# Optimization experiments

Hardware: AMD Instinct MI355X
Metric: run time of the kernel (lower is better)

The kernel has to match this reference:

```python
import jax, jax.numpy as jnp
import numpy as np

N = 200000   # total atoms in batched graph
E = 3200000  # total bonds (directed edges)
B = 512      # number of graphs / sequences
L = 1000     # miRNA sequence length


def _gcn(x, W, b, src, dst, dis):
    # PyG GCNConv: add self-loops, symmetric normalization D^-1/2 A D^-1/2
    h = x @ W                                   # [N, Fout]
    msg = (dis[src] * dis[dst])[:, None] * h[src]
    agg = jax.ops.segment_sum(msg, dst, num_segments=x.shape[0])
    return agg + (dis * dis)[:, None] * h + b   # self-loop term + bias


def _conv1d(x, k, b):
    # x: [B, C, L], k: [O, I, K]  (torch Conv1d, VALID padding)
    y = jax.lax.conv_general_dilated(x, k, (1,), 'VALID',
                                     dimension_numbers=('NCH', 'OIH', 'NCH'))
    return y + b[None, :, None]


def _mp3(x):
    # torch MaxPool1d(3): window 3, stride 3, floor
    return jax.lax.reduce_window(x, -jnp.inf, jax.lax.max, (1, 1, 3), (1, 1, 3), 'VALID')


def setup_inputs() -> dict:
    key = jax.random.key(0)
    ks = jax.random.split(key, 24)
    w = lambda k, s: (jax.random.normal(k, s, jnp.float32) * 0.1)
    p = {}
    p['x'] = jax.random.normal(ks[0], (N, 4), jnp.float32)
    p['edge_index'] = jax.random.randint(ks[1], (2, E), 0, N, jnp.int32)
    p['batch'] = (jnp.arange(N, dtype=jnp.int32) * B // N).astype(jnp.int32)  # every graph non-empty
    p['target'] = jax.random.normal(ks[2], (B, L, 5), jnp.float32)
    # GCN layers 4->4->8->16
    p['W1'] = w(ks[3], (4, 4));    p['b1'] = jnp.zeros(4, jnp.float32)
    p['W2'] = w(ks[4], (4, 8));    p['b2'] = jnp.zeros(8, jnp.float32)
    p['W3'] = w(ks[5], (8, 16));   p['b3'] = jnp.zeros(16, jnp.float32)
    p['Wg1'] = w(ks[6], (16, 1024)); p['bg1'] = jnp.zeros(1024, jnp.float32)
    p['Wg2'] = w(ks[7], (1024, 128)); p['bg2'] = jnp.zeros(128, jnp.float32)
    # CNN stack on sequences, kernels [O, I, 8]
    p['K1'] = w(ks[8], (32, 5, 8));   p['cb1'] = jnp.zeros(32, jnp.float32)
    p['K2'] = w(ks[9], (64, 32, 8));  p['cb2'] = jnp.zeros(64, jnp.float32)
    p['K3'] = w(ks[10], (128, 64, 8)); p['cb3'] = jnp.zeros(128, jnp.float32)
    p['Wxt'] = w(ks[11], (128, 128)); p['bxt'] = jnp.zeros(128, jnp.float32)
    # fusion head
    p['Wf1'] = w(ks[12], (256, 1024)); p['bf1'] = jnp.zeros(1024, jnp.float32)
    p['Wf2'] = w(ks[13], (1024, 512)); p['bf2'] = jnp.zeros(512, jnp.float32)
    p['Wo'] = w(ks[14], (512, 2));     p['bo'] = jnp.zeros(2, jnp.float32)
    return p


def reference(x, edge_index, batch, target, W1, b1, W2, b2, W3, b3,
              Wg1, bg1, Wg2, bg2, K1, cb1, K2, cb2, K3, cb3,
              Wxt, bxt, Wf1, bf1, Wf2, bf2, Wo, bo):
    src, dst = edge_index[0], edge_index[1]
    deg = jax.ops.segment_sum(jnp.ones(src.shape[0], x.dtype), dst,
                              num_segments=x.shape[0]) + 1.0  # +1 self-loop
    dis = jax.lax.rsqrt(deg)
    # Graph branch (dropout is identity in eval)
    h = jax.nn.relu(_gcn(x, W1, b1, src, dst, dis))
    h = jax.nn.relu(_gcn(h, W2, b2, src, dst, dis))
    h = jax.nn.relu(_gcn(h, W3, b3, src, dst, dis))
    g = jax.ops.segment_max(h, batch, num_segments=B)  # global_max_pool
    g = jax.nn.relu(g @ Wg1 + bg1)
    g = g @ Wg2 + bg2
    # Sequence branch
    t = jnp.transpose(target, (0, 2, 1))  # [B, 5, L]
    c = _mp3(jax.nn.relu(_conv1d(t, K1, cb1)))
    c = _mp3(jax.nn.relu(_conv1d(c, K2, cb2)))
    c = _mp3(jax.nn.relu(_conv1d(c, K3, cb3)))
    c = jnp.mean(c, axis=2)               # [B, 128]
    c = jax.nn.relu(c @ Wxt + bxt)
    # Fusion head
    xc = jnp.concatenate([g, c], axis=1)  # [B, 256]
    xc = jax.nn.relu(xc @ Wf1 + bf1)
    xc = jax.nn.relu(xc @ Wf2 + bf2)
    return xc @ Wo + bo                    # [B, 2]
```

## Files before the change

### kernel.cpp

```cpp
#include <hip/hip_runtime.h>
#include <hip/hip_fp16.h>
#include <cstddef>

#define NA 200000
#define NE 3200000
#define NB 512
#define NBKT 256
#define BKTN 782
#define BKTCAP 16384
#define NEPB 3200

typedef _Float16 hv2 __attribute__((ext_vector_type(2)));
typedef _Float16 half8 __attribute__((ext_vector_type(8)));
typedef float floatx4 __attribute__((ext_vector_type(4)));
union UH2 { unsigned u; __half2 h; hv2 v; };
__device__ __forceinline__ float4 h4f(unsigned a, unsigned b) {
    UH2 x, y; x.u = a; y.u = b;
    float2 fa = __half22float2(x.h), fb = __half22float2(y.h);
    return make_float4(fa.x, fa.y, fb.x, fb.y);
}
__device__ __forceinline__ unsigned f2h(float a, float b) {
    UH2 r; r.h = __float22half2_rn(make_float2(a, b));
    return r.u;
}

__global__ void k_init(unsigned* g, int* gcursor,
                       float* gvec, const float* __restrict__ bg2,
                       float* xf2, const float* __restrict__ bf2,
                       float* xf1, const float* __restrict__ bf1,
                       const float* __restrict__ K2, const float* __restrict__ K3,
                       __half* __restrict__ Wt2, __half* __restrict__ Wt3) {
    int i = blockIdx.x * blockDim.x + threadIdx.x;
    if (i < NB * 16) g[i] = 0u;
    if (i < NBKT) gcursor[i] = i * BKTCAP;
    if (i < NB * 128) gvec[i] = bg2[i & 127];
    if (i < NB * 512) xf2[i] = bf2[i & 511];
    if (i < NB * 1024) xf1[i] = bf1[i & 1023];
    if (i < 64 * 32 * 8) {
        int o = i >> 8, rem = i & 255, c = rem >> 3, kk = rem & 7;
        Wt2[(o << 8) + (kk << 5) + c] = __float2half(K2[i]);
    }
    if (i < 128 * 64 * 8) {
        int o = i >> 9, rem = i & 511, c = rem >> 3, kk = rem & 7;
        Wt3[(o << 9) + (kk << 6) + c] = __float2half(K3[i]);
    }
}

template<int CIN, int COUT, int OBLK, int LIN, int PITCH, int POUT, int NTT>
__device__ __forceinline__ void dev_conv1(int b, int oy,
        const float* __restrict__ in, const float* __restrict__ Kw,
        const float* __restrict__ bias, __half* __restrict__ out) {
    constexpr int SPO = 256 / OBLK;
    constexpr int PT = (NTT < 4) ? NTT : 4;
    constexpr int NPASS = (NTT + PT - 1) / PT;
    __shared__ __align__(16) float s_in[CIN * PITCH];
    for (int idx = threadIdx.x; idx < CIN * PITCH; idx += 256) s_in[idx] = 0.f;
    __syncthreads();
    for (int idx = threadIdx.x; idx < LIN * CIN; idx += 256) {
        int p = idx / CIN, c = idx - p * CIN;
        s_in[c * PITCH + p] = in[(size_t)b * (LIN * CIN) + idx];
    }
    __syncthreads();
    int ol = threadIdx.x / SPO;
    int s  = threadIdx.x - ol * SPO;
    int o  = oy * OBLK + ol;
    float bo = bias[o];
    const float* wrow = Kw + (size_t)o * CIN * 8;
    for (int pass = 0; pass < NPASS; pass++) {
        float acc[PT][12];
#pragma unroll
        for (int tt = 0; tt < PT; tt++)
#pragma unroll
            for (int j = 0; j < 12; j++) acc[tt][j] = 0.f;
        bool vld[PT]; int tgs[PT];
#pragma unroll
        for (int tt = 0; tt < PT; tt++) {
            int ta = pass * PT + tt;
            int tg = s + SPO * ta;
            tgs[tt] = tg;
            vld[tt] = (ta < NTT) && (4 * tg < POUT);
        }
        for (int i = 0; i < CIN; i++) {
            float wa[8];
            const float4* wp = (const float4*)(wrow + (size_t)i * 8);
            *(float4*)&wa[0] = wp[0];
            *(float4*)&wa[4] = wp[1];
#pragma unroll
            for (int tt = 0; tt < PT; tt++) {
                if (vld[tt]) {
                    const float4* xr = (const float4*)&s_in[i * PITCH + 12 * tgs[tt]];
                    float xa[20];
#pragma unroll
                    for (int q = 0; q < 5; q++) *(float4*)&xa[4 * q] = xr[q];
#pragma unroll
                    for (int j = 0; j < 12; j++) {
                        float sm = acc[tt][j];
#pragma unroll
                        for (int k = 0; k < 8; k++) sm = fmaf(xa[j + k], wa[k], sm);
                        acc[tt][j] = sm;
                    }
                }
            }
        }
#pragma unroll
        for (int tt = 0; tt < PT; tt++) {
            if (vld[tt]) {
#pragma unroll
                for (int p = 0; p < 4; p++) {
                    int P = 4 * tgs[tt] + p;
                    if (P < POUT) {
                        float m = fmaxf(fmaxf(acc[tt][3 * p], acc[tt][3 * p + 1]), acc[tt][3 * p + 2]);
                        out[((size_t)b * COUT + o) * POUT + P] = __float2half(fmaxf(m + bo, 0.f));
                    }
                }
            }
        }
    }
}

__device__ __forceinline__ void dev_conv2_mfma(int b,
        const __half* __restrict__ pool1, const __half* __restrict__ Wt2,
        const float* __restrict__ cb2, __half* __restrict__ pool2t,
        char* smem) {
    __half* sT   = (__half*)smem;
    __half* outS = (__half*)smem;
    const __half* inp = pool1 + (size_t)b * (32 * 331);
    for (int idx = threadIdx.x; idx < 32 * 331; idx += 256) {
        int c = idx / 331;
        int p = idx - c * 331;
        sT[p * 40 + c] = inp[idx];
    }
    __syncthreads();
    int lane = threadIdx.x & 63, wv = threadIdx.x >> 6;
    int l15 = lane & 15, lg = lane >> 4;
    int mtBeg = wv * 5;
    int nmt = (wv == 3) ? 6 : 5;
    const floatx4 FZ = {0.f, 0.f, 0.f, 0.f};
    floatx4 acc[6][4];
#pragma unroll
    for (int mi = 0; mi < 6; mi++)
#pragma unroll
        for (int nt = 0; nt < 4; nt++) acc[mi][nt] = FZ;
    const half8* WB = (const half8*)Wt2;
    for (int s = 0; s < 8; s++) {
        half8 bfr[4];
#pragma unroll
        for (int nt = 0; nt < 4; nt++)
            bfr[nt] = WB[(nt * 16 + l15) * 32 + s * 4 + lg];
        half8 afr[6];
#pragma unroll
        for (int mi = 0; mi < 6; mi++) {
            if (mi < nmt) {
                int row = (mtBeg + mi) * 16 + l15 + s;
                afr[mi] = *(const half8*)(sT + row * 40 + lg * 8);
            }
        }
#pragma unroll
        for (int mi = 0; mi < 6; mi++) {
            if (mi < nmt) {
#pragma unroll
                for (int nt = 0; nt < 4; nt++)
                    acc[mi][nt] = __builtin_amdgcn_mfma_f32_16x16x32_f16(
                        afr[mi], bfr[nt], acc[mi][nt], 0, 0, 0);
            }
        }
    }
    __syncthreads();
    float bo[4];
#pragma unroll
    for (int nt = 0; nt < 4; nt++) bo[nt] = cb2[nt * 16 + l15];
#pragma unroll
    for (int mi = 0; mi < 6; mi++) {
        if (mi < nmt) {
#pragma unroll
            for (int nt = 0; nt < 4; nt++) {
                int o = nt * 16 + l15;
#pragma unroll
                for (int r = 0; r < 4; r++) {
                    int p = (mtBeg + mi) * 16 + lg * 4 + r;
                    float v = fmaxf(acc[mi][nt][r] + bo[nt], 0.f);
                    outS[p * 68 + o] = __float2half(v);
                }
            }
        }
    }
    __syncthreads();
    __half* op = pool2t + (size_t)b * (108 * 64);
    for (int idx = threadIdx.x; idx < 108 * 64; idx += 256) {
        int P = idx >> 6, o = idx & 63;
        float v0 = __half2float(outS[(3 * P) * 68 + o]);
        float v1 = __half2float(outS[(3 * P + 1) * 68 + o]);
        float v2 = __half2float(outS[(3 * P + 2) * 68 + o]);
        op[idx] = __float2half(fmaxf(fmaxf(v0, v1), v2));
    }
}

__device__ __forceinline__ void dev_conv3_mfma(int b,
        const __half* __restrict__ pool2t, const __half* __restrict__ Wt3,
        const float* __restrict__ cb3, float* __restrict__ pool3,
        char* smem) {
    __half* sT  = (__half*)smem;
    float* outS = (float*)smem;
    const uint4* inp = (const uint4*)(pool2t + (size_t)b * (108 * 64));
    for (int t = threadIdx.x; t < 108 * 8; t += 256) {
        int r = t >> 3, s8 = t & 7;
        *(uint4*)(sT + r * 72 + s8 * 8) = inp[t];
    }
    __syncthreads();
    int lane = threadIdx.x & 63, wv = threadIdx.x >> 6;
    int l15 = lane & 15, lg = lane >> 4;
    int mtBeg = wv * 2;
    int nmt = (wv == 3) ? 1 : 2;
    const floatx4 FZ = {0.f, 0.f, 0.f, 0.f};
    floatx4 acc[2][8];
#pragma unroll
    for (int mi = 0; mi < 2; mi++)
#pragma unroll
        for (int nt = 0; nt < 8; nt++) acc[mi][nt] = FZ;
    const half8* WB = (const half8*)Wt3;
    for (int s = 0; s < 16; s++) {
        half8 bfr[8];
#pragma unroll
        for (int nt = 0; nt < 8; nt++)
            bfr[nt] = WB[(nt * 16 + l15) * 64 + s * 4 + lg];
        half8 afr[2];
#pragma unroll
        for (int mi = 0; mi < 2; mi++) {
            if (mi < nmt) {
                int row = (mtBeg + mi) * 16 + l15 + (s >> 1);
                afr[mi] = *(const half8*)(sT + row * 72 + (s & 1) * 32 + lg * 8);
            }
        }
#pragma unroll
        for (int mi = 0; mi < 2; mi++) {
            if (mi < nmt) {
#pragma unroll
                for (int nt = 0; nt < 8; nt++)
                    acc[mi][nt] = __builtin_amdgcn_mfma_f32_16x16x32_f16(
                        afr[mi], bfr[nt], acc[mi][nt], 0, 0, 0);
            }
        }
    }
    __syncthreads();
    float bo[8];
#pragma unroll
    for (int nt = 0; nt < 8; nt++) bo[nt] = cb3[nt * 16 + l15];
#pragma unroll
    for (int mi = 0; mi < 2; mi++) {
        if (mi < nmt) {
#pragma unroll
            for (int nt = 0; nt < 8; nt++) {
                int o = nt * 16 + l15;
#pragma unroll
                for (int r = 0; r < 4; r++) {
                    int p = (mtBeg + mi) * 16 + lg * 4 + r;
                    if (p < 100)
                        outS[p * 132 + o] = fmaxf(acc[mi][nt][r] + bo[nt], 0.f);
                }
            }
        }
    }
    __syncthreads();
    float* op = pool3 + (size_t)b * (128 * 33);
    for (int idx = threadIdx.x; idx < 128 * 33; idx += 256) {
        int o = idx / 33, P = idx - o * 33;
        float v0 = outS[(3 * P) * 132 + o];
        float v1 = outS[(3 * P + 1) * 132 + o];
        float v2 = outS[(3 * P + 2) * 132 + o];
        op[idx] = fmaxf(fmaxf(v0, v1), v2);
    }
}

__global__ __launch_bounds__(256) void k_A(
        const int* __restrict__ src, const int* __restrict__ dst,
        int* __restrict__ gcursor, unsigned* __restrict__ stage,
        const float* __restrict__ tgt, const float* __restrict__ K1,
        const float* __restrict__ cb1, __half* __restrict__ pool1) {
    __shared__ int hcnt[NBKT];
    __shared__ int hbase[NBKT];
    int bx = blockIdx.x;
    if (bx >= 1000) {
        dev_conv1<5, 32, 16, 1000, 1008, 331, 6>(bx - 1000, 0, tgt, K1, cb1, pool1);
        return;
    }
    int e0 = bx * NEPB;
    hcnt[threadIdx.x] = 0;
    __syncthreads();
    const int4* d4 = (const int4*)(dst + e0);
    for (int i = threadIdx.x; i < NEPB / 4; i += 256) {
        int4 d = d4[i];
        atomicAdd(&hcnt[d.x / BKTN], 1);
        atomicAdd(&hcnt[d.y / BKTN], 1);
        atomicAdd(&hcnt[d.z / BKTN], 1);
        atomicAdd(&hcnt[d.w / BKTN], 1);
    }
    __syncthreads();
    hbase[threadIdx.x] = atomicAdd(&gcursor[threadIdx.x], hcnt[threadIdx.x]);
    hcnt[threadIdx.x] = 0;
    __syncthreads();
    const int4* s4 = (const int4*)(src + e0);
    for (int i = threadIdx.x; i < NEPB / 4; i += 256) {
        int4 d = d4[i];
        int4 s = s4[i];
        int ds[4] = {d.x, d.y, d.z, d.w};
        int ss[4] = {s.x, s.y, s.z, s.w};
#pragma unroll
        for (int j = 0; j < 4; j++) {
            int bkt = ds[j] / BKTN;
            int dloc = ds[j] - bkt * BKTN;
            int k = atomicAdd(&hcnt[bkt], 1);
            stage[hbase[bkt] + k] = ((unsigned)dloc << 18) | (unsigned)ss[j];
        }
    }
}

__global__ __launch_bounds__(256) void k_Bp(
        const unsigned* __restrict__ stage, const int* __restrict__ gcursor,
        int* __restrict__ rowptr, int* __restrict__ cnt, int* __restrict__ csr,
        const float* __restrict__ x, float4* __restrict__ dt1,
        const float* __restrict__ tgt, const float* __restrict__ K1,
        const float* __restrict__ cb1, __half* __restrict__ pool1) {
    __shared__ int lcnt[BKTN];
    __shared__ int lpos[BKTN];
    __shared__ int partial[256];
    __shared__ int sbase;
    int bx = blockIdx.x;
    if (bx >= NBKT) {
        dev_conv1<5, 32, 16, 1000, 1008, 331, 6>(bx - NBKT, 1, tgt, K1, cb1, pool1);
        return;
    }
    int t = threadIdx.x;
    int bkt = bx;
    int tot = gcursor[t] - t * BKTCAP;
    partial[t] = tot;
    __syncthreads();
#pragma unroll
    for (int off = 1; off < 256; off <<= 1) {
        int u = (t >= off) ? partial[t - off] : 0;
        __syncthreads();
        partial[t] += u;
        __syncthreads();
    }
    if (t == 0) sbase = (bkt == 0) ? 0 : partial[bkt - 1];
    __syncthreads();
    int base = sbase;
    int n0 = bkt * BKTN;
    int ncnt = (NA - n0 < BKTN) ? (NA - n0) : BKTN;
    int eBeg = bkt * BKTCAP;
    int eCnt = gcursor[bkt] - eBeg;
    for (int i = t; i < BKTN; i += 256) lcnt[i] = 0;
    __syncthreads();
    for (int i = t; i < eCnt; i += 256)
        atomicAdd(&lcnt[stage[eBeg + i] >> 18], 1);
    __syncthreads();
    int mysum = 0;
#pragma unroll
    for (int j = 0; j < 4; j++) {
        int node = 4 * t + j;
        if (node < ncnt) mysum += lcnt[node];
    }
    partial[t] = mysum;
    __syncthreads();
#pragma unroll
    for (int off = 1; off < 256; off <<= 1) {
        int u = (t >= off) ? partial[t - off] : 0;
        __syncthreads();
        partial[t] += u;
        __syncthreads();
    }
    int running = partial[t] - mysum;
#pragma unroll
    for (int j = 0; j < 4; j++) {
        int node = 4 * t + j;
        if (node < ncnt) {
            lpos[node] = running;
            rowptr[n0 + node] = base + running;
            cnt[n0 + node] = lcnt[node];
            running += lcnt[node];
        }
    }
    __syncthreads();
    for (int i = t; i < eCnt; i += 256) {
        unsigned v = stage[eBeg + i];
        int dloc = v >> 18;
        int s = v & 0x3FFFF;
        int k = atomicAdd(&lpos[dloc], 1);
        csr[base + k] = s;
    }
    for (int i = t; i < ncnt; i += 256) {
        int n = n0 + i;
        float4 p = ((const float4*)x)[n];
        float dv = rsqrtf((float)lcnt[i] + 1.0f);
        dt1[n] = make_float4(dv * p.x, dv * p.y, dv * p.z, dv * p.w);
    }
}

__global__ __launch_bounds__(256) void k_B(
        const __half* __restrict__ pool1, const __half* __restrict__ Wt2,
        const float* __restrict__ cb2, __half* __restrict__ pool2t,
        const float4* __restrict__ dt1, const int* __restrict__ rowptr,
        const int* __restrict__ cnt, const int* __restrict__ csr,
        const float* __restrict__ W1, const float* __restrict__ b1,
        float4* __restrict__ dt2) {
    __shared__ __align__(16) char smem[45696];
    int bx = blockIdx.x;
    if (bx < 512) {
        dev_conv2_mfma(bx, pool1, Wt2, cb2, pool2t, smem);
        return;
    }
    __shared__ float sW[16];
    if (threadIdx.x < 16) sW[threadIdx.x] = W1[threadIdx.x];
    __syncthreads();
    int n = (bx - 512) * 256 + threadIdx.x;
    if (n >= NA) return;
    int cn = cnt[n];
    float dv = rsqrtf((float)cn + 1.0f);
    const int* row = csr + rowptr[n];
    float4 acc = dt1[n];
    int e = 0;
    for (; e + 3 < cn; e += 4) {
        int i0 = row[e], i1 = row[e + 1], i2 = row[e + 2], i3 = row[e + 3];
        float4 v0 = dt1[i0], v1 = dt1[i1], v2 = dt1[i2], v3 = dt1[i3];
        acc.x += (v0.x + v1.x) + (v2.x + v3.x);
        acc.y += (v0.y + v1.y) + (v2.y + v3.y);
        acc.z += (v0.z + v1.z) + (v2.z + v3.z);
        acc.w += (v0.w + v1.w) + (v2.w + v3.w);
    }
    for (; e < cn; e++) {
        float4 v = dt1[row[e]];
        acc.x += v.x; acc.y += v.y; acc.z += v.z; acc.w += v.w;
    }
    const float4 bq = *(const float4*)b1;
    float a[4] = {acc.x, acc.y, acc.z, acc.w};
    float bb[4] = {bq.x, bq.y, bq.z, bq.w};
    float o[4];
#pragma unroll
    for (int f = 0; f < 4; f++) {
        float s = 0.f;
#pragma unroll
        for (int k = 0; k < 4; k++) s = fmaf(a[k], sW[k * 4 + f], s);
        o[f] = dv * fmaxf(fmaf(dv, s, bb[f]), 0.f);
    }
    dt2[n] = make_float4(o[0], o[1], o[2], o[3]);
}

__global__ __launch_bounds__(256) void k_C(
        const __half* __restrict__ pool2t, const __half* __restrict__ Wt3,
        const float* __restrict__ cb3, float* __restrict__ pool3,
        const float4* __restrict__ dt2, const int* __restrict__ rowptr,
        const int* __restrict__ cnt, const int* __restrict__ csr,
        const float* __restrict__ W2, const float* __restrict__ b2,
        uint4* __restrict__ dt3) {
    __shared__ __align__(16) char smem[52800];
    int bx = blockIdx.x;
    if (bx < 512) {
        dev_conv3_mfma(bx, pool2t, Wt3, cb3, pool3, smem);
        return;
    }
    __shared__ float sW[32];
    if (threadIdx.x < 32) sW[threadIdx.x] = W2[threadIdx.x];
    __syncthreads();
    int n = (bx - 512) * 256 + threadIdx.x;
    if (n >= NA) return;
    int cn = cnt[n];
    float dv = rsqrtf((float)cn + 1.0f);
    const int* row = csr + rowptr[n];
    float4 acc = dt2[n];
    int e = 0;
    for (; e + 3 < cn; e += 4) {
        int i0 = row[e], i1 = row[e + 1], i2 = row[e + 2], i3 = row[e + 3];
        float4 v0 = dt2[i0], v1 = dt2[i1], v2 = dt2[i2], v3 = dt2[i3];
        acc.x += (v0.x + v1.x) + (v2.x + v3.x);
        acc.y += (v0.y + v1.y) + (v2.y + v3.y);
        acc.z += (v0.z + v1.z) + (v2.z + v3.z);
        acc.w += (v0.w + v1.w) + (v2.w + v3.w);
    }
    for (; e < cn; e++) {
        float4 v = dt2[row[e]];
        acc.x += v.x; acc.y += v.y; acc.z += v.z; acc.w += v.w;
    }
    float a[4] = {acc.x, acc.y, acc.z, acc.w};
    float o[8];
#pragma unroll
    for (int f = 0; f < 8; f++) {
        float s = 0.f;
#pragma unroll
        for (int k = 0; k < 4; k++) s = fmaf(a[k], sW[k * 8 + f], s);
        o[f] = dv * fmaxf(fmaf(dv, s, b2[f]), 0.f);
    }
    dt3[n] = make_uint4(f2h(o[0], o[1]), f2h(o[2], o[3]),
                        f2h(o[4], o[5]), f2h(o[6], o[7]));
}

__global__ __launch_bounds__(256) void k_D(
        const uint4* __restrict__ dt3, const int* __restrict__ rowptr,
        const int* __restrict__ cnt, const int* __restrict__ csr,
        const float* __restrict__ W3, const float* __restrict__ b3,
        const int* __restrict__ batch, unsigned* __restrict__ g,
        const float* __restrict__ pool3, const float* __restrict__ Wxt,
        const float* __restrict__ bxt, float* __restrict__ cx) {
    int bx = blockIdx.x;
    if (bx >= 782) {
        __shared__ float sa[8 * 128];
        int b0 = (bx - 782) * 8;
        for (int t = threadIdx.x; t < 8 * 128; t += 256) {
            int gg = t >> 7, k = t & 127;
            const float* r = pool3 + ((size_t)(b0 + gg) * 128 + k) * 33;
            float s = 0.f;
#pragma unroll
            for (int p = 0; p < 33; p++) s += r[p];
            sa[t] = s * (1.f / 33.f);
        }
        __syncthreads();
        int j = threadIdx.x;
        if (j >= 128) return;
        float bj = bxt[j];
        float acc[8];
#pragma unroll
        for (int gg = 0; gg < 8; gg++) acc[gg] = bj;
#pragma unroll 4
        for (int k = 0; k < 128; k++) {
            float w = Wxt[(size_t)k * 128 + j];
#pragma unroll
            for (int gg = 0; gg < 8; gg++) acc[gg] = fmaf(sa[gg * 128 + k], w, acc[gg]);
        }
#pragma unroll
        for (int gg = 0; gg < 8; gg++)
            cx[(size_t)(b0 + gg) * 128 + j] = fmaxf(acc[gg], 0.f);
        return;
    }
    __shared__ float sW[128];
    __shared__ unsigned sg[32];
    __shared__ int sbmin;
    int id = bx;
    if (threadIdx.x < 128) sW[threadIdx.x] = W3[threadIdx.x];
    if (threadIdx.x < 32) sg[threadIdx.x] = 0u;
    if (threadIdx.x == 0) sbmin = batch[id * 256];
    __syncthreads();
    int n = id * 256 + threadIdx.x;
    if (n < NA) {
        int cn = cnt[n];
        float dv = rsqrtf((float)cn + 1.0f);
        const int* row = csr + rowptr[n];
        uint4 sv = dt3[n];
        float4 lo = h4f(sv.x, sv.y), hi = h4f(sv.z, sv.w);
        float a0 = lo.x, a1 = lo.y, a2 = lo.z, a3 = lo.w;
        float a4 = hi.x, a5 = hi.y, a6 = hi.z, a7 = hi.w;
        int e = 0;
        for (; e + 3 < cn; e += 4) {
            uint4 p0 = dt3[row[e]],     p1 = dt3[row[e + 1]];
            uint4 p2 = dt3[row[e + 2]], p3 = dt3[row[e + 3]];
            float4 l0 = h4f(p0.x, p0.y), h0 = h4f(p0.z, p0.w);
            float4 l1 = h4f(p1.x, p1.y), h1 = h4f(p1.z, p1.w);
            float4 l2 = h4f(p2.x, p2.y), h2 = h4f(p2.z, p2.w);
            float4 l3 = h4f(p3.x, p3.y), h3v = h4f(p3.z, p3.w);
            a0 += (l0.x + l1.x) + (l2.x + l3.x);
            a1 += (l0.y + l1.y) + (l2.y + l3.y);
            a2 += (l0.z + l1.z) + (l2.z + l3.z);
            a3 += (l0.w + l1.w) + (l2.w + l3.w);
            a4 += (h0.x + h1.x) + (h2.x + h3v.x);
            a5 += (h0.y + h1.y) + (h2.y + h3v.y);
            a6 += (h0.z + h1.z) + (h2.z + h3v.z);
            a7 += (h0.w + h1.w) + (h2.w + h3v.w);
        }
        for (; e < cn; e++) {
            uint4 p = dt3[row[e]];
            float4 l = h4f(p.x, p.y), h = h4f(p.z, p.w);
            a0 += l.x; a1 += l.y; a2 += l.z; a3 += l.w;
            a4 += h.x; a5 += h.y; a6 += h.z; a7 += h.w;
        }
        float af[8] = {a0, a1, a2, a3, a4, a5, a6, a7};
        int rb = batch[n] - sbmin;
        if (rb > 1) rb = 1;
#pragma unroll
        for (int f = 0; f < 16; f++) {
            float s = 0.f;
#pragma unroll
            for (int k = 0; k < 8; k++) s = fmaf(af[k], sW[k * 16 + f], s);
            float r = fmaxf(fmaf(dv, s, b3[f]), 0.f);
            atomicMax(&sg[rb * 16 + f], __float_as_uint(r));
        }
    }
    __syncthreads();
    if (threadIdx.x < 32) {
        unsigned v = sg[threadIdx.x];
        int rb2 = threadIdx.x >> 4, f = threadIdx.x & 15;
        int bbn = sbmin + rb2;
        if (v != 0u && bbn < NB) atomicMax(&g[bbn * 16 + f], v);
    }
}

__global__ __launch_bounds__(256) void k_head_g(
        const float* __restrict__ g, const float* __restrict__ Wg1,
        const float* __restrict__ bg1, float* __restrict__ gp1) {
    __shared__ float sa[8 * 16];
    int bx = blockIdx.x;
    int b0 = (bx >> 2) * 8;
    if (threadIdx.x < 128)
        sa[threadIdx.x] = g[b0 * 16 + threadIdx.x];
    __syncthreads();
    int j = (bx & 3) * 256 + threadIdx.x;
    float bj = bg1[j];
    float acc[8];
#pragma unroll
    for (int gg = 0; gg < 8; gg++) acc[gg] = bj;
#pragma unroll
    for (int k = 0; k < 16; k++) {
        float w = Wg1[(size_t)k * 1024 + j];
#pragma unroll
        for (int gg = 0; gg < 8; gg++) acc[gg] = fmaf(sa[gg * 16 + k], w, acc[gg]);
    }
#pragma unroll
    for (int gg = 0; gg < 8; gg++)
        gp1[(size_t)(b0 + gg) * 1024 + j] = fmaxf(acc[gg], 0.f);
}

__global__ __launch_bounds__(256) void k_gvec_ks(
        const float* __restrict__ gp1, const float* __restrict__ Wg2,
        float* __restrict__ gvec) {
    __shared__ float sa[8 * 128];
    int k0 = blockIdx.x * 128;
    int b0 = blockIdx.y * 8;
    for (int t = threadIdx.x; t < 8 * 128; t += 256) {
        int gg = t >> 7, k = t & 127;
        sa[t] = gp1[(size_t)(b0 + gg) * 1024 + k0 + k];
    }
    __syncthreads();
    int j  = threadIdx.x & 127;
    int kh = (threadIdx.x >> 7) * 64;
    const float* Wp = Wg2 + (size_t)(k0 + kh) * 128 + j;
    float acc[8];
#pragma unroll
    for (int gg = 0; gg < 8; gg++) acc[gg] = 0.f;
    for (int k = 0; k < 64; k += 16) {
        float w[16];
#pragma unroll
        for (int u = 0; u < 16; u++) w[u] = Wp[(size_t)(k + u) * 128];
#pragma unroll
        for (int u = 0; u < 16; u++) {
#pragma unroll
            for (int gg = 0; gg < 8; gg++)
                acc[gg] = fmaf(sa[gg * 128 + kh + k + u], w[u], acc[gg]);
        }
    }
#pragma unroll
    for (int gg = 0; gg < 8; gg++)
        atomicAdd(&gvec[(size_t)(b0 + gg) * 128 + j], acc[gg]);
}

__global__ __launch_bounds__(256) void k_cat2(
        const float* __restrict__ gvec, const float* __restrict__ cx,
        const float* __restrict__ Wf1, float* __restrict__ xf1) {
    __shared__ float sa[8 * 128];
    int jx = blockIdx.x & 3;
    int kh = blockIdx.x >> 2;
    int b0 = blockIdx.y * 8;
    const float* A = kh ? cx : gvec;
    for (int t = threadIdx.x; t < 8 * 128; t += 256) {
        int gg = t >> 7, k = t & 127;
        sa[t] = A[(size_t)(b0 + gg) * 128 + k];
    }
    __syncthreads();
    int j = jx * 256 + threadIdx.x;
    const float* Wp = Wf1 + (size_t)(kh * 128) * 1024 + j;
    float acc[8];
#pragma unroll
    for (int gg = 0; gg < 8; gg++) acc[gg] = 0.f;
    for (int k = 0; k < 128; k += 16) {
        float w[16];
#pragma unroll
        for (int u = 0; u < 16; u++) w[u] = Wp[(size_t)(k + u) * 1024];
#pragma unroll
        for (int u = 0; u < 16; u++) {
#pragma unroll
            for (int gg = 0; gg < 8; gg++)
                acc[gg] = fmaf(sa[gg * 128 + k + u], w[u], acc[gg]);
        }
    }
#pragma unroll
    for (int gg = 0; gg < 8; gg++)
        atomicAdd(&xf1[(size_t)(b0 + gg) * 1024 + j], acc[gg]);
}

__global__ __launch_bounds__(256) void k_xf2_ks(
        const float* __restrict__ xf1, const float* __restrict__ Wf2,
        float* __restrict__ xf2) {
    __shared__ float sa[8 * 256];
    int jb = blockIdx.x & 1;
    int k0 = (blockIdx.x >> 1) * 256;
    int b0 = blockIdx.y * 8;
    for (int t = threadIdx.x; t < 8 * 256; t += 256) {
        int gg = t >> 8, k = t & 255;
        sa[t] = fmaxf(xf1[(size_t)(b0 + gg) * 1024 + k0 + k], 0.f);
    }
    __syncthreads();
    int j = jb * 256 + threadIdx.x;
    const float* Wp = Wf2 + (size_t)k0 * 512 + j;
    float acc[8];
#pragma unroll
    for (int gg = 0; gg < 8; gg++) acc[gg] = 0.f;
    for (int k = 0; k < 256; k += 16) {
        float w[16];
#pragma unroll
        for (int u = 0; u < 16; u++) w[u] = Wp[(size_t)(k + u) * 512];
#pragma unroll
        for (int u = 0; u < 16; u++) {
#pragma unroll
            for (int gg = 0; gg < 8; gg++)
                acc[gg] = fmaf(sa[gg * 256 + k + u], w[u], acc[gg]);
        }
    }
#pragma unroll
    for (int gg = 0; gg < 8; gg++)
        atomicAdd(&xf2[(size_t)(b0 + gg) * 512 + j], acc[gg]);
}

__global__ __launch_bounds__(256) void k_dense_out(
        const float* __restrict__ A, const float* __restrict__ W,
        const float* __restrict__ bias, float* __restrict__ out) {
    int idx = blockIdx.x * 256 + threadIdx.x;
    if (idx >= NB * 2) return;
    int b = idx >> 1, j = idx & 1;
    float s = bias[j];
    const float4* A4 = (const float4*)(A + (size_t)b * 512);
    for (int k4 = 0; k4 < 128; k4 += 8) {
        float4 av[8];
#pragma unroll
        for (int u = 0; u < 8; u++) av[u] = A4[k4 + u];
#pragma unroll
        for (int u = 0; u < 8; u++) {
            int kb = (k4 + u) * 4;
            s = fmaf(fmaxf(av[u].x, 0.f), W[(kb + 0) * 2 + j], s);
            s = fmaf(fmaxf(av[u].y, 0.f), W[(kb + 1) * 2 + j], s);
            s = fmaf(fmaxf(av[u].z, 0.f), W[(kb + 2) * 2 + j], s);
            s = fmaf(fmaxf(av[u].w, 0.f), W[(kb + 3) * 2 + j], s);
        }
    }
    out[idx] = s;
}

extern "C" void kernel_launch(void* const* d_in, const int* in_sizes, int n_in,
                              void* d_out, int out_size, void* d_ws, size_t ws_size,
                              hipStream_t stream) {
    (void)in_sizes; (void)n_in; (void)out_size; (void)ws_size;
    const float* x   = (const float*)d_in[0];
    const int*  ei   = (const int*)d_in[1];
    const int*  batch= (const int*)d_in[2];
    const float* tgt = (const float*)d_in[3];
    const float* W1  = (const float*)d_in[4];  const float* b1  = (const float*)d_in[5];
    const float* W2  = (const float*)d_in[6];  const float* b2  = (const float*)d_in[7];
    const float* W3  = (const float*)d_in[8];  const float* b3  = (const float*)d_in[9];
    const float* Wg1 = (const float*)d_in[10]; const float* bg1 = (const float*)d_in[11];
    const float* Wg2 = (const float*)d_in[12]; const float* bg2 = (const float*)d_in[13];
    const float* K1  = (const float*)d_in[14]; const float* cb1 = (const float*)d_in[15];
    const float* K2  = (const float*)d_in[16]; const float* cb2 = (const float*)d_in[17];
    const float* K3  = (const float*)d_in[18]; const float* cb3 = (const float*)d_in[19];
    const float* Wxt = (const float*)d_in[20]; const float* bxt = (const float*)d_in[21];
    const float* Wf1 = (const float*)d_in[22]; const float* bf1 = (const float*)d_in[23];
    const float* Wf2 = (const float*)d_in[24]; const float* bf2 = (const float*)d_in[25];
    const float* Wo  = (const float*)d_in[26]; const float* bo  = (const float*)d_in[27];
    const int* srcp = ei;
    const int* dstp = ei + NE;

    float* ws = (float*)d_ws;
    float4* dt1 = (float4*)ws; ws += (size_t)NA * 4;
    float4* dt2 = (float4*)ws; ws += (size_t)NA * 4;
    uint4*  dt3 = (uint4*)ws;  ws += (size_t)NA * 4;
    float* g     = ws; ws += NB * 16;
    float* gp1   = ws; ws += NB * 1024;
    float* gvec  = ws; ws += NB * 128;
    float* cx    = ws; ws += NB * 128;
    float* xf1   = ws; ws += NB * 1024;
    float* xf2   = ws; ws += NB * 512;
    __half* pool1 = (__half*)ws; ws += (size_t)NB * 32 * 331;
    __half* pool2t = (__half*)ws; ws += (size_t)NB * 64 * 108;
    float* pool3 = ws; ws += (size_t)NB * 128 * 33;
    __half* Wt2 = (__half*)ws; ws += 64 * 256 / 2;
    __half* Wt3 = (__half*)ws; ws += 128 * 512 / 2;
    int*   cnt    = (int*)ws; ws += NA;
    int*   rowptr = (int*)ws; ws += NA;
    int*   csr    = (int*)ws; ws += NE;
    int*   gcursor= (int*)ws; ws += NBKT;
    unsigned* stage = (unsigned*)ws; ws += (size_t)NBKT * BKTCAP;

    dim3 blk(256);

    k_init<<<2048, blk, 0, stream>>>((unsigned*)g, gcursor, gvec, bg2, xf2, bf2,
                                     xf1, bf1, K2, K3, Wt2, Wt3);
    k_A<<<1512, blk, 0, stream>>>(srcp, dstp, gcursor, stage, tgt, K1, cb1, pool1);
    k_Bp<<<768, blk, 0, stream>>>(stage, gcursor, rowptr, cnt, csr, x, dt1,
                                  tgt, K1, cb1, pool1);
    k_B<<<1294, blk, 0, stream>>>(pool1, Wt2, cb2, pool2t,
                                  dt1, rowptr, cnt, csr, W1, b1, dt2);
    k_C<<<1294, blk, 0, stream>>>(pool2t, Wt3, cb3, pool3,
                                  dt2, rowptr, cnt, csr, W2, b2, dt3);
    k_D<<<846, blk, 0, stream>>>(dt3, rowptr, cnt, csr, W3, b3,
                                 batch, (unsigned*)g, pool3, Wxt, bxt, cx);

    k_head_g<<<256, blk, 0, stream>>>(g, Wg1, bg1, gp1);
    k_gvec_ks<<<dim3(8, 64), blk, 0, stream>>>(gp1, Wg2, gvec);
    k_cat2<<<dim3(8, 64), blk, 0, stream>>>(gvec, cx, Wf1, xf1);
    k_xf2_ks<<<dim3(8, 64), blk, 0, stream>>>(xf1, Wf2, xf2);
    k_dense_out<<<4, blk, 0, stream>>>(xf2, Wo, bo, (float*)d_out);
}
```

Before: 430.0 us.

## Stage edge bucketing in LDS for coalesced writes; unroll CSR gathers by eight

```diff
diff --git a/kernel.cpp b/kernel.cpp
--- a/kernel.cpp
+++ b/kernel.cpp
@@ -49,11 +49,11 @@
 template<int CIN, int COUT, int OBLK, int LIN, int PITCH, int POUT, int NTT>
 __device__ __forceinline__ void dev_conv1(int b, int oy,
         const float* __restrict__ in, const float* __restrict__ Kw,
-        const float* __restrict__ bias, __half* __restrict__ out) {
+        const float* __restrict__ bias, __half* __restrict__ out,
+        float* s_in) {
     constexpr int SPO = 256 / OBLK;
     constexpr int PT = (NTT < 4) ? NTT : 4;
     constexpr int NPASS = (NTT + PT - 1) / PT;
-    __shared__ __align__(16) float s_in[CIN * PITCH];
     for (int idx = threadIdx.x; idx < CIN * PITCH; idx += 256) s_in[idx] = 0.f;
     __syncthreads();
     for (int idx = threadIdx.x; idx < LIN * CIN; idx += 256) {
@@ -276,18 +276,24 @@
         int* __restrict__ gcursor, unsigned* __restrict__ stage,
         const float* __restrict__ tgt, const float* __restrict__ K1,
         const float* __restrict__ cb1, __half* __restrict__ pool1) {
-    __shared__ int hcnt[NBKT];
-    __shared__ int hbase[NBKT];
+    __shared__ __align__(16) char smem[20160];
     int bx = blockIdx.x;
     if (bx >= 1000) {
-        dev_conv1<5, 32, 16, 1000, 1008, 331, 6>(bx - 1000, 0, tgt, K1, cb1, pool1);
+        dev_conv1<5, 32, 16, 1000, 1008, 331, 6>(bx - 1000, 0, tgt, K1, cb1,
+                                                 pool1, (float*)smem);
         return;
     }
+    int* hcnt  = (int*)smem;
+    int* hbase = hcnt + 256;
+    int* lbase = hbase + 256;
+    unsigned* sbuf = (unsigned*)(lbase + 256);
+    unsigned char* sbkt = (unsigned char*)(sbuf + NEPB);
+    int t = threadIdx.x;
     int e0 = bx * NEPB;
-    hcnt[threadIdx.x] = 0;
+    hcnt[t] = 0;
     __syncthreads();
     const int4* d4 = (const int4*)(dst + e0);
-    for (int i = threadIdx.x; i < NEPB / 4; i += 256) {
+    for (int i = t; i < NEPB / 4; i += 256) {
         int4 d = d4[i];
         atomicAdd(&hcnt[d.x / BKTN], 1);
         atomicAdd(&hcnt[d.y / BKTN], 1);
@@ -295,11 +301,21 @@
         atomicAdd(&hcnt[d.w / BKTN], 1);
     }
     __syncthreads();
-    hbase[threadIdx.x] = atomicAdd(&gcursor[threadIdx.x], hcnt[threadIdx.x]);
-    hcnt[threadIdx.x] = 0;
+    int myc = hcnt[t];
+    hbase[t] = atomicAdd(&gcursor[t], myc);
+    __syncthreads();
+#pragma unroll
+    for (int off = 1; off < 256; off <<= 1) {
+        int u = (t >= off) ? hcnt[t - off] : 0;
+        __syncthreads();
+        hcnt[t] += u;
+        __syncthreads();
+    }
+    lbase[t] = hcnt[t] - myc;
+    hcnt[t] = 0;
     __syncthreads();
     const int4* s4 = (const int4*)(src + e0);
-    for (int i = threadIdx.x; i < NEPB / 4; i += 256) {
+    for (int i = t; i < NEPB / 4; i += 256) {
         int4 d = d4[i];
         int4 s = s4[i];
         int ds[4] = {d.x, d.y, d.z, d.w};
@@ -309,8 +325,16 @@
             int bkt = ds[j] / BKTN;
             int dloc = ds[j] - bkt * BKTN;
             int k = atomicAdd(&hcnt[bkt], 1);
-            stage[hbase[bkt] + k] = ((unsigned)dloc << 18) | (unsigned)ss[j];
-        }
+            int pos = lbase[bkt] + k;
+            sbuf[pos] = ((unsigned)dloc << 18) | (unsigned)ss[j];
+            sbkt[pos] = (unsigned char)bkt;
+        }
+    }
+    __syncthreads();
+    for (int i = t; i < NEPB; i += 256) {
+        unsigned v = sbuf[i];
+        int bkt = sbkt[i];
+        stage[hbase[bkt] + (i - lbase[bkt])] = v;
     }
 }
 
@@ -320,15 +344,17 @@
         const float* __restrict__ x, float4* __restrict__ dt1,
         const float* __restrict__ tgt, const float* __restrict__ K1,
         const float* __restrict__ cb1, __half* __restrict__ pool1) {
-    __shared__ int lcnt[BKTN];
-    __shared__ int lpos[BKTN];
-    __shared__ int partial[256];
+    __shared__ __align__(16) char smem[20160];
     __shared__ int sbase;
     int bx = blockIdx.x;
     if (bx >= NBKT) {
-        dev_conv1<5, 32, 16, 1000, 1008, 331, 6>(bx - NBKT, 1, tgt, K1, cb1, pool1);
+        dev_conv1<5, 32, 16, 1000, 1008, 331, 6>(bx - NBKT, 1, tgt, K1, cb1,
+                                                 pool1, (float*)smem);
         return;
     }
+    int* lcnt    = (int*)smem;
+    int* lpos    = lcnt + BKTN;
+    int* partial = lpos + BKTN;
     int t = threadIdx.x;
     int bkt = bx;
     int tot = gcursor[t] - t * BKTCAP;
@@ -418,13 +444,17 @@
     const int* row = csr + rowptr[n];
     float4 acc = dt1[n];
     int e = 0;
-    for (; e + 3 < cn; e += 4) {
-        int i0 = row[e], i1 = row[e + 1], i2 = row[e + 2], i3 = row[e + 3];
-        float4 v0 = dt1[i0], v1 = dt1[i1], v2 = dt1[i2], v3 = dt1[i3];
-        acc.x += (v0.x + v1.x) + (v2.x + v3.x);
-        acc.y += (v0.y + v1.y) + (v2.y + v3.y);
-        acc.z += (v0.z + v1.z) + (v2.z + v3.z);
-        acc.w += (v0.w + v1.w) + (v2.w + v3.w);
+    for (; e + 7 < cn; e += 8) {
+        int idx[8];
+#pragma unroll
+        for (int u = 0; u < 8; u++) idx[u] = row[e + u];
+        float4 v[8];
+#pragma unroll
+        for (int u = 0; u < 8; u++) v[u] = dt1[idx[u]];
+#pragma unroll
+        for (int u = 0; u < 8; u++) {
+            acc.x += v[u].x; acc.y += v[u].y; acc.z += v[u].z; acc.w += v[u].w;
+        }
     }
     for (; e < cn; e++) {
         float4 v = dt1[row[e]];
@@ -467,13 +497,17 @@
     const int* row = csr + rowptr[n];
     float4 acc = dt2[n];
     int e = 0;
-    for (; e + 3 < cn; e += 4) {
-        int i0 = row[e], i1 = row[e + 1], i2 = row[e + 2], i3 = row[e + 3];
-        float4 v0 = dt2[i0], v1 = dt2[i1], v2 = dt2[i2], v3 = dt2[i3];
-        acc.x += (v0.x + v1.x) + (v2.x + v3.x);
-        acc.y += (v0.y + v1.y) + (v2.y + v3.y);
-        acc.z += (v0.z + v1.z) + (v2.z + v3.z);
-        acc.w += (v0.w + v1.w) + (v2.w + v3.w);
+    for (; e + 7 < cn; e += 8) {
+        int idx[8];
+#pragma unroll
+        for (int u = 0; u < 8; u++) idx[u] = row[e + u];
+        float4 v[8];
+#pragma unroll
+        for (int u = 0; u < 8; u++) v[u] = dt2[idx[u]];
+#pragma unroll
+        for (int u = 0; u < 8; u++) {
+            acc.x += v[u].x; acc.y += v[u].y; acc.z += v[u].z; acc.w += v[u].w;
+        }
     }
     for (; e < cn; e++) {
         float4 v = dt2[row[e]];
```

Result: faster. 420.0 us (-2.3%).
